# Performance work log

Measured on AMD Instinct MI355X. Metric: run time of the kernel, lower is better.

Reference implementation:

```python
import jax, jax.numpy as jnp
import numpy as np

EMBED_DIM = 768
NUM_HEADS = 12
HEAD_DIM = EMBED_DIM // NUM_HEADS


def setup_inputs() -> dict:
    key = jax.random.key(0)
    k1, k2, k3 = jax.random.split(key, 3)
    B, T = 128, 128
    x = jax.random.normal(k1, (B, T, EMBED_DIM), dtype=jnp.float32)
    # weights stored as [in, out] so forward is x @ W (equivalent to torch Linear, bias=False)
    w_qkv = jax.random.normal(k2, (EMBED_DIM, 3 * EMBED_DIM), dtype=jnp.float32) * (EMBED_DIM ** -0.5)
    w_proj = jax.random.normal(k3, (EMBED_DIM, EMBED_DIM), dtype=jnp.float32) * (EMBED_DIM ** -0.5)
    return {"x": x, "w_qkv": w_qkv, "w_proj": w_proj}


def reference(x, w_qkv, w_proj):
    B, T, C = x.shape
    # fused QKV projection -> (3, B, H, T, D)
    qkv = (x @ w_qkv).reshape(B, T, 3, NUM_HEADS, HEAD_DIM)
    q, k, v = jnp.transpose(qkv, (2, 0, 3, 1, 4))
    # scaled dot-product scores (B, H, T, T)
    att = jnp.einsum('bhqd,bhkd->bhqk', q, k) * (HEAD_DIM ** -0.5)
    causal = jnp.tril(jnp.ones((T, T), dtype=bool))
    att = jnp.where(causal, att, -jnp.inf)
    # float32 softmax then cast back (matches att.float().softmax().to(x.dtype))
    att = jax.nn.softmax(att.astype(jnp.float32), axis=-1).astype(x.dtype)
    # dropout is identity in eval/reference mode
    out = jnp.einsum('bhqk,bhkd->bhqd', att, v)          # (B, H, T, D)
    out = jnp.transpose(out, (0, 2, 1, 3)).reshape(B, T, C)
    return out @ w_proj
```

## Files before the change

kernel.cpp:

```cpp
#include <hip/hip_runtime.h>

typedef __bf16 bf16_t;
typedef bf16_t bf16x8 __attribute__((ext_vector_type(8)));
typedef bf16_t bf16x4 __attribute__((ext_vector_type(4)));
typedef float f32x4 __attribute__((ext_vector_type(4)));

__device__ __forceinline__ f32x4 mfma16(bf16x8 a, bf16x8 b, f32x4 c) {
  return __builtin_amdgcn_mfma_f32_16x16x32_bf16(a, b, c, 0, 0, 0);
}

__device__ __forceinline__ void gload16(const bf16_t* g, bf16_t* l) {
  __builtin_amdgcn_global_load_lds(
      (const __attribute__((address_space(1))) void*)g,
      (__attribute__((address_space(3))) void*)l, 16, 0, 0);
}

__global__ void prep_kernel(const float* __restrict__ x, const float* __restrict__ wq,
                            const float* __restrict__ wp, bf16_t* __restrict__ xb,
                            bf16_t* __restrict__ wqt, bf16_t* __restrict__ wpt) {
  __shared__ bf16_t tile[32][33];
  const int bid = blockIdx.x;
  if (bid < 12288) {
    int i = bid * 256 + threadIdx.x;
    float4 v = ((const float4*)x)[i];
    bf16x4 o;
    o[0] = (bf16_t)v.x; o[1] = (bf16_t)v.y; o[2] = (bf16_t)v.z; o[3] = (bf16_t)v.w;
    *(bf16x4*)&xb[(size_t)i * 4] = o;
    return;
  }
  const int t = bid - 12288;
  const int ty = t / 96, txb = t % 96;
  const float* in;
  bf16_t* out;
  int N, n0;
  if (txb < 72) { in = wq; out = wqt; N = 2304; n0 = txb * 32; }
  else          { in = wp; out = wpt; N = 768;  n0 = (txb - 72) * 32; }
  const int k0 = ty * 32;
  const int tx = threadIdx.x & 31, tyy = threadIdx.x >> 5;
#pragma unroll
  for (int ph = 0; ph < 4; ++ph) {
    int k = tyy + ph * 8;
    tile[k][tx] = (bf16_t)in[(size_t)(k0 + k) * N + n0 + tx];
  }
  __syncthreads();
#pragma unroll
  for (int ph = 0; ph < 4; ++ph) {
    int n = tyy + ph * 8;
    out[(size_t)(n0 + n) * 768 + k0 + tx] = tile[tx][n];
  }
}

template <int BN, bool F32OUT>
__global__ __launch_bounds__(256, 3) void gemm_persist(
    const bf16_t* __restrict__ A, const bf16_t* __restrict__ Bt,
    void* __restrict__ Cout, int N, int K, int nbn, int q, int r) {
  constexpr int NQ = BN / 32;
  __shared__ bf16_t As[2][128 * 64];
  __shared__ bf16_t Bs[2][BN * 64];
  const int tid = threadIdx.x;
  const int lane = tid & 63;
  const int w = tid >> 6;
  const int wm = w >> 1, wn = w & 1;
  const int lr = lane & 15, kg = lane >> 4;

  const int G = gridDim.x;
  const int bid = blockIdx.x;
  const int lb = (bid & 7) * (G >> 3) + (bid >> 3);
  int nj, start;
  if (lb < r) { nj = q + 1; start = lb * (q + 1); }
  else        { nj = q;     start = r * (q + 1) + (lb - r) * q; }

  const int NKT = K >> 6;
  const int sr = tid >> 3, sslot = tid & 7;

  auto stage = [&](int buf, const bf16_t* Aj, const bf16_t* Bj, int k0) {
#pragma unroll
    for (int it = 0; it < 4; ++it) {
      int rr = it * 32 + sr;
      gload16(Aj + (size_t)rr * K + (k0 + ((sslot ^ (rr & 7)) << 3)),
              &As[buf][(it * 256 + tid) * 8]);
    }
#pragma unroll
    for (int it = 0; it < NQ; ++it) {
      int rr = it * 32 + sr;
      gload16(Bj + (size_t)rr * K + (k0 + ((sslot ^ (rr & 7)) << 3)),
              &Bs[buf][(it * 256 + tid) * 8]);
    }
  };

  int job = start;
  int bm = job / nbn, bn = job % nbn;
  const bf16_t* Aj = A + (size_t)bm * 128 * K;
  const bf16_t* Bj = Bt + (size_t)bn * BN * K;
  stage(0, Aj, Bj, 0);
  __syncthreads();
  int buf = 0;

  for (int j = 0; j < nj; ++j) {
    f32x4 acc[4][NQ];
#pragma unroll
    for (int i = 0; i < 4; ++i)
#pragma unroll
      for (int n = 0; n < NQ; ++n) acc[i][n] = (f32x4){0.f, 0.f, 0.f, 0.f};

    int nbm = 0, nbnx = 0;
    const bf16_t *nAj = nullptr, *nBj = nullptr;
    if (j + 1 < nj) {
      int njob = job + 1;
      nbm = njob / nbn; nbnx = njob % nbn;
      nAj = A + (size_t)nbm * 128 * K;
      nBj = Bt + (size_t)nbnx * BN * K;
    }

    for (int kt = 0; kt < NKT; ++kt) {
      if (kt + 1 < NKT)      stage(buf ^ 1, Aj, Bj, (kt + 1) << 6);
      else if (j + 1 < nj)   stage(buf ^ 1, nAj, nBj, 0);
#pragma unroll
      for (int kk = 0; kk < 2; ++kk) {
        const int slot = ((kk << 2) + kg) ^ (lr & 7);
        bf16x8 af[4], bfv[NQ];
#pragma unroll
        for (int mq = 0; mq < 4; ++mq) {
          int rr = wm * 64 + mq * 16 + lr;
          af[mq] = *(const bf16x8*)&As[buf][(rr << 6) + (slot << 3)];
        }
#pragma unroll
        for (int nq = 0; nq < NQ; ++nq) {
          int rr = wn * (BN / 2) + nq * 16 + lr;
          bfv[nq] = *(const bf16x8*)&Bs[buf][(rr << 6) + (slot << 3)];
        }
#pragma unroll
        for (int mq = 0; mq < 4; ++mq)
#pragma unroll
          for (int nq = 0; nq < NQ; ++nq)
            acc[mq][nq] = mfma16(af[mq], bfv[nq], acc[mq][nq]);
      }
      __syncthreads();
      buf ^= 1;
    }

    const int row0 = bm * 128 + wm * 64 + kg * 4;
    const int col0 = bn * BN + wn * (BN / 2) + lr;
#pragma unroll
    for (int mq = 0; mq < 4; ++mq)
#pragma unroll
      for (int nq = 0; nq < NQ; ++nq)
#pragma unroll
        for (int rr = 0; rr < 4; ++rr) {
          size_t idx = (size_t)(row0 + mq * 16 + rr) * N + (col0 + nq * 16);
          if constexpr (F32OUT)
            ((float*)Cout)[idx] = acc[mq][nq][rr];
          else
            ((bf16_t*)Cout)[idx] = (bf16_t)acc[mq][nq][rr];
        }

    job++; bm = nbm; bn = nbnx; Aj = nAj; Bj = nBj;
  }
}

#define ATT_H 12
__global__ __launch_bounds__(256, 2) void attn_kernel(const bf16_t* __restrict__ qkv,
                                                      bf16_t* __restrict__ obuf) {
  __shared__ bf16_t Ks[128 * 72];
  __shared__ bf16_t Vt[64 * 136];
  __shared__ bf16_t Ps[128 * 136];
  const int tid = threadIdx.x, lane = tid & 63, w = tid >> 6;
  const int lr = lane & 15, kg = lane >> 4;
  const int bh = blockIdx.x;
  const int b = bh / ATT_H, h = bh % ATT_H;
  const size_t base = (size_t)b * 128 * 2304;
  const int hoff = h * 64;

#pragma unroll
  for (int it = 0; it < 4; ++it) {
    int idx = it * 256 + tid;
    int r = idx >> 3, slot = idx & 7;
    bf16x8 v = *(const bf16x8*)&qkv[base + (size_t)r * 2304 + 768 + hoff + slot * 8];
    *(bf16x8*)&Ks[r * 72 + slot * 8] = v;
  }
#pragma unroll 4
  for (int it = 0; it < 32; ++it) {
    int idx = it * 256 + tid;
    int t = idx >> 6, d = idx & 63;
    Vt[d * 136 + t] = qkv[base + (size_t)t * 2304 + 1536 + hoff + d];
  }
  const int qrow0 = w * 32;
  bf16x8 qf[2][2];
#pragma unroll
  for (int mt = 0; mt < 2; ++mt)
#pragma unroll
    for (int kk = 0; kk < 2; ++kk)
      qf[mt][kk] = *(const bf16x8*)&qkv[base + (size_t)(qrow0 + mt * 16 + lr) * 2304 + hoff +
                                        kk * 32 + kg * 8];
  __syncthreads();

  const int NT = 2 * w + 2;
  f32x4 acc[2][8];
#pragma unroll
  for (int mt = 0; mt < 2; ++mt)
#pragma unroll
    for (int nt = 0; nt < 8; ++nt) acc[mt][nt] = (f32x4){0.f, 0.f, 0.f, 0.f};

#pragma unroll
  for (int nt = 0; nt < 8; ++nt) {
    if (nt < NT) {
#pragma unroll
      for (int kk = 0; kk < 2; ++kk) {
        bf16x8 kf = *(const bf16x8*)&Ks[(nt * 16 + lr) * 72 + kk * 32 + kg * 8];
        acc[0][nt] = mfma16(qf[0][kk], kf, acc[0][nt]);
        acc[1][nt] = mfma16(qf[1][kk], kf, acc[1][nt]);
      }
    }
  }

#pragma unroll
  for (int mt = 0; mt < 2; ++mt) {
#pragma unroll
    for (int rr = 0; rr < 4; ++rr) {
      const int row = qrow0 + mt * 16 + kg * 4 + rr;
      float m = -1e30f;
#pragma unroll
      for (int nt = 0; nt < 8; ++nt) {
        if (nt < NT) {
          int col = nt * 16 + lr;
          float s = acc[mt][nt][rr] * 0.125f;
          s = (col <= row) ? s : -1e30f;
          acc[mt][nt][rr] = s;
          m = fmaxf(m, s);
        }
      }
      m = fmaxf(m, __shfl_xor(m, 1));
      m = fmaxf(m, __shfl_xor(m, 2));
      m = fmaxf(m, __shfl_xor(m, 4));
      m = fmaxf(m, __shfl_xor(m, 8));
      float ssum = 0.f;
#pragma unroll
      for (int nt = 0; nt < 8; ++nt) {
        if (nt < NT) {
          float p = __builtin_amdgcn_exp2f((acc[mt][nt][rr] - m) * 1.44269504f);
          acc[mt][nt][rr] = p;
          ssum += p;
        }
      }
      ssum += __shfl_xor(ssum, 1);
      ssum += __shfl_xor(ssum, 2);
      ssum += __shfl_xor(ssum, 4);
      ssum += __shfl_xor(ssum, 8);
      float inv = 1.0f / ssum;
#pragma unroll
      for (int nt = 0; nt < 8; ++nt) {
        if (nt < NT) Ps[row * 136 + nt * 16 + lr] = (bf16_t)(acc[mt][nt][rr] * inv);
      }
    }
  }

  f32x4 oacc[2][4];
#pragma unroll
  for (int mt = 0; mt < 2; ++mt)
#pragma unroll
    for (int dt = 0; dt < 4; ++dt) oacc[mt][dt] = (f32x4){0.f, 0.f, 0.f, 0.f};

  const int KS = w + 1;
#pragma unroll
  for (int ks = 0; ks < 4; ++ks) {
    if (ks < KS) {
      bf16x8 pa0 = *(const bf16x8*)&Ps[(qrow0 + lr) * 136 + ks * 32 + kg * 8];
      bf16x8 pa1 = *(const bf16x8*)&Ps[(qrow0 + 16 + lr) * 136 + ks * 32 + kg * 8];
#pragma unroll
      for (int dt = 0; dt < 4; ++dt) {
        bf16x8 vb = *(const bf16x8*)&Vt[(dt * 16 + lr) * 136 + ks * 32 + kg * 8];
        oacc[0][dt] = mfma16(pa0, vb, oacc[0][dt]);
        oacc[1][dt] = mfma16(pa1, vb, oacc[1][dt]);
      }
    }
  }

#pragma unroll
  for (int mt = 0; mt < 2; ++mt)
#pragma unroll
    for (int dt = 0; dt < 4; ++dt)
#pragma unroll
      for (int rr = 0; rr < 4; ++rr) {
        int t = qrow0 + mt * 16 + kg * 4 + rr;
        obuf[((size_t)b * 128 + t) * 768 + hoff + dt * 16 + lr] = (bf16_t)oacc[mt][dt][rr];
      }
}

extern "C" void kernel_launch(void* const* d_in, const int* in_sizes, int n_in,
                              void* d_out, int out_size, void* d_ws, size_t ws_size,
                              hipStream_t stream) {
  const float* x = (const float*)d_in[0];
  const float* w_qkv = (const float*)d_in[1];
  const float* w_proj = (const float*)d_in[2];
  float* out = (float*)d_out;
  char* ws = (char*)d_ws;

  bf16_t* xb     = (bf16_t*)(ws);
  bf16_t* wqkvt  = (bf16_t*)(ws + 25165824);
  bf16_t* wprojt = (bf16_t*)(ws + 28704768);
  bf16_t* qkv    = (bf16_t*)(ws + 29884416);
  bf16_t* obuf   = (bf16_t*)(ws + 105381888);

  prep_kernel<<<dim3(12288 + 2304), dim3(256), 0, stream>>>(x, w_qkv, w_proj, xb, wqkvt, wprojt);
  gemm_persist<128, false><<<dim3(512), dim3(256), 0, stream>>>(
      xb, wqkvt, (void*)qkv, 2304, 768, 18, 4, 256);
  attn_kernel<<<dim3(1536), dim3(256), 0, stream>>>(qkv, obuf);
  gemm_persist<64, true><<<dim3(768), dim3(256), 0, stream>>>(
      obuf, wprojt, (void*)out, 768, 768, 12, 2, 0);
}
```

Before: 157.9 us.

## Replace double-buffered GEMMs with 3-stage LDS ring and per-block A-row reuse

Both GEMMs now use a single kernel with a three-slot LDS ring buffer and a prefetch distance of two stages. The loads are tracked with explicit vmcnt waits and a single barrier per k-step, replacing the two syncthreads of the previous double buffer. Each block keeps one 128-row A panel and walks several consecutive 64-wide N tiles, so A stays cache-resident and the job schedule is simpler. The QKV GEMM changes from 128-wide to 64-wide N tiles, and occupancy drops to 2 blocks per CU. This trades fewer barriers and deeper prefetch for lower per-tile B reuse.

```diff
diff --git a/kernel.cpp b/kernel.cpp
--- a/kernel.cpp
+++ b/kernel.cpp
@@ -14,6 +14,14 @@
       (const __attribute__((address_space(1))) void*)g,
       (__attribute__((address_space(3))) void*)l, 16, 0, 0);
 }
+
+#define BARRIER()                      \
+  do {                                 \
+    asm volatile("" ::: "memory");     \
+    __builtin_amdgcn_s_barrier();      \
+    asm volatile("" ::: "memory");     \
+  } while (0)
+#define VMCNT(n) asm volatile("s_waitcnt vmcnt(" #n ")" ::: "memory")
 
 __global__ void prep_kernel(const float* __restrict__ x, const float* __restrict__ wq,
                             const float* __restrict__ wp, bf16_t* __restrict__ xb,
@@ -50,13 +58,13 @@
   }
 }
 
-template <int BN, bool F32OUT>
-__global__ __launch_bounds__(256, 3) void gemm_persist(
+template <bool F32OUT>
+__global__ __launch_bounds__(256, 2) void gemm_ring(
     const bf16_t* __restrict__ A, const bf16_t* __restrict__ Bt,
-    void* __restrict__ Cout, int N, int K, int nbn, int q, int r) {
-  constexpr int NQ = BN / 32;
-  __shared__ bf16_t As[2][128 * 64];
-  __shared__ bf16_t Bs[2][BN * 64];
+    void* __restrict__ Cout, int N, int nbn, int jpb) {
+  constexpr int K = 768;
+  constexpr int NKT = 12;
+  __shared__ bf16_t ring[3][12288];
   const int tid = threadIdx.x;
   const int lane = tid & 63;
   const int w = tid >> 6;
@@ -66,85 +74,82 @@
   const int G = gridDim.x;
   const int bid = blockIdx.x;
   const int lb = (bid & 7) * (G >> 3) + (bid >> 3);
-  int nj, start;
-  if (lb < r) { nj = q + 1; start = lb * (q + 1); }
-  else        { nj = q;     start = r * (q + 1) + (lb - r) * q; }
-
-  const int NKT = K >> 6;
-  const int sr = tid >> 3, sslot = tid & 7;
-
-  auto stage = [&](int buf, const bf16_t* Aj, const bf16_t* Bj, int k0) {
+  const int start = lb * jpb;
+  const int bm = start / nbn;
+  const int bn0 = start % nbn;
+  const bf16_t* Ab = A + (size_t)bm * 128 * K;
+  const int S = jpb * NKT;
+
+  auto stageS = [&](int s) {
+    if (s >= S) return;
+    const int jb = s / NKT;
+    const int kt = s - jb * NKT;
+    const int k0 = kt << 6;
+    const bf16_t* Bj = Bt + (size_t)(bn0 + jb) * 64 * K;
+    bf16_t* L = &ring[kt % 3][0];
 #pragma unroll
     for (int it = 0; it < 4; ++it) {
-      int rr = it * 32 + sr;
-      gload16(Aj + (size_t)rr * K + (k0 + ((sslot ^ (rr & 7)) << 3)),
-              &As[buf][(it * 256 + tid) * 8]);
-    }
-#pragma unroll
-    for (int it = 0; it < NQ; ++it) {
-      int rr = it * 32 + sr;
-      gload16(Bj + (size_t)rr * K + (k0 + ((sslot ^ (rr & 7)) << 3)),
-              &Bs[buf][(it * 256 + tid) * 8]);
+      int c = it * 256 + tid;
+      int r = c >> 3, p = c & 7;
+      gload16(Ab + (size_t)r * K + (k0 + ((p ^ (r & 7)) << 3)), L + c * 8);
+    }
+#pragma unroll
+    for (int it = 0; it < 2; ++it) {
+      int c = it * 256 + tid;
+      int r = c >> 3, p = c & 7;
+      gload16(Bj + (size_t)r * K + (k0 + ((p ^ (r & 7)) << 3)), L + 8192 + c * 8);
     }
   };
 
-  int job = start;
-  int bm = job / nbn, bn = job % nbn;
-  const bf16_t* Aj = A + (size_t)bm * 128 * K;
-  const bf16_t* Bj = Bt + (size_t)bn * BN * K;
-  stage(0, Aj, Bj, 0);
-  __syncthreads();
-  int buf = 0;
-
-  for (int j = 0; j < nj; ++j) {
-    f32x4 acc[4][NQ];
+  stageS(0);
+  stageS(1);
+
+  for (int j = 0; j < jpb; ++j) {
+    f32x4 acc[4][2];
 #pragma unroll
     for (int i = 0; i < 4; ++i)
 #pragma unroll
-      for (int n = 0; n < NQ; ++n) acc[i][n] = (f32x4){0.f, 0.f, 0.f, 0.f};
-
-    int nbm = 0, nbnx = 0;
-    const bf16_t *nAj = nullptr, *nBj = nullptr;
-    if (j + 1 < nj) {
-      int njob = job + 1;
-      nbm = njob / nbn; nbnx = njob % nbn;
-      nAj = A + (size_t)nbm * 128 * K;
-      nBj = Bt + (size_t)nbnx * BN * K;
-    }
+      for (int n = 0; n < 2; ++n) acc[i][n] = (f32x4){0.f, 0.f, 0.f, 0.f};
+
+    const int sbase = j * NKT;
+    const bool lastj = (j == jpb - 1);
 
     for (int kt = 0; kt < NKT; ++kt) {
-      if (kt + 1 < NKT)      stage(buf ^ 1, Aj, Bj, (kt + 1) << 6);
-      else if (j + 1 < nj)   stage(buf ^ 1, nAj, nBj, 0);
+      if (lastj && kt == NKT - 1) { VMCNT(0); } else { VMCNT(6); }
+      BARRIER();
+      stageS(sbase + kt + 2);
+
+      const bf16_t* L = &ring[kt % 3][0];
 #pragma unroll
       for (int kk = 0; kk < 2; ++kk) {
-        const int slot = ((kk << 2) + kg) ^ (lr & 7);
-        bf16x8 af[4], bfv[NQ];
+        const int q = (kk << 2) + kg;
+        const int ph = q ^ (lr & 7);
+        bf16x8 af[4], bfv[2];
 #pragma unroll
         for (int mq = 0; mq < 4; ++mq) {
-          int rr = wm * 64 + mq * 16 + lr;
-          af[mq] = *(const bf16x8*)&As[buf][(rr << 6) + (slot << 3)];
-        }
-#pragma unroll
-        for (int nq = 0; nq < NQ; ++nq) {
-          int rr = wn * (BN / 2) + nq * 16 + lr;
-          bfv[nq] = *(const bf16x8*)&Bs[buf][(rr << 6) + (slot << 3)];
+          int r = wm * 64 + mq * 16 + lr;
+          af[mq] = *(const bf16x8*)&L[r * 64 + ph * 8];
+        }
+#pragma unroll
+        for (int nq = 0; nq < 2; ++nq) {
+          int r = wn * 32 + nq * 16 + lr;
+          bfv[nq] = *(const bf16x8*)&L[8192 + r * 64 + ph * 8];
         }
 #pragma unroll
         for (int mq = 0; mq < 4; ++mq)
 #pragma unroll
-          for (int nq = 0; nq < NQ; ++nq)
+          for (int nq = 0; nq < 2; ++nq)
             acc[mq][nq] = mfma16(af[mq], bfv[nq], acc[mq][nq]);
       }
-      __syncthreads();
-      buf ^= 1;
-    }
-
+    }
+
+    const int bn = bn0 + j;
     const int row0 = bm * 128 + wm * 64 + kg * 4;
-    const int col0 = bn * BN + wn * (BN / 2) + lr;
+    const int col0 = bn * 64 + wn * 32 + lr;
 #pragma unroll
     for (int mq = 0; mq < 4; ++mq)
 #pragma unroll
-      for (int nq = 0; nq < NQ; ++nq)
+      for (int nq = 0; nq < 2; ++nq)
 #pragma unroll
         for (int rr = 0; rr < 4; ++rr) {
           size_t idx = (size_t)(row0 + mq * 16 + rr) * N + (col0 + nq * 16);
@@ -153,8 +158,6 @@
           else
             ((bf16_t*)Cout)[idx] = (bf16_t)acc[mq][nq][rr];
         }
-
-    job++; bm = nbm; bn = nbnx; Aj = nAj; Bj = nBj;
   }
 }
 
@@ -302,9 +305,7 @@
   bf16_t* obuf   = (bf16_t*)(ws + 105381888);
 
   prep_kernel<<<dim3(12288 + 2304), dim3(256), 0, stream>>>(x, w_qkv, w_proj, xb, wqkvt, wprojt);
-  gemm_persist<128, false><<<dim3(512), dim3(256), 0, stream>>>(
-      xb, wqkvt, (void*)qkv, 2304, 768, 18, 4, 256);
+  gemm_ring<false><<<dim3(512), dim3(256), 0, stream>>>(xb, wqkvt, (void*)qkv, 2304, 36, 9);
   attn_kernel<<<dim3(1536), dim3(256), 0, stream>>>(qkv, obuf);
-  gemm_persist<64, true><<<dim3(768), dim3(256), 0, stream>>>(
-      obuf, wprojt, (void*)out, 768, 768, 12, 2, 0);
-}
+  gemm_ring<true><<<dim3(512), dim3(256), 0, stream>>>(obuf, wprojt, (void*)out, 768, 12, 3);
+}
```

Result: no change. 157.2 us (-0.4%).

## Replace syncthreads with raw barriers and vmcnt waits in persistent GEMMs

Applied to the files above, without the earlier changes.

Both persistent GEMMs now use a flat step counter over jobs and k-tiles. Each step issues the next stage's async global-to-LDS loads between raw s_barrier calls and waits only on the older batch through an explicit vmcnt count, instead of relying on __syncthreads to drain everything. The intent is to let the prefetch overlap the MFMA work and to cut the full memory drain at each k-step. K is also made a compile-time constant, and the QKV GEMM's occupancy hint drops from 3 to 2 blocks per CU. The hand-written vmcnt values assume exact load counts per stage, and two barriers per step add sync overhead.

```diff
diff --git a/kernel.cpp b/kernel.cpp
--- a/kernel.cpp
+++ b/kernel.cpp
@@ -14,6 +14,14 @@
       (const __attribute__((address_space(1))) void*)g,
       (__attribute__((address_space(3))) void*)l, 16, 0, 0);
 }
+
+#define BARRIER()                      \
+  do {                                 \
+    asm volatile("" ::: "memory");     \
+    __builtin_amdgcn_s_barrier();      \
+    asm volatile("" ::: "memory");     \
+  } while (0)
+#define VMCNT(n) asm volatile("s_waitcnt vmcnt(" #n ")" ::: "memory")
 
 __global__ void prep_kernel(const float* __restrict__ x, const float* __restrict__ wq,
                             const float* __restrict__ wp, bf16_t* __restrict__ xb,
@@ -50,10 +58,12 @@
   }
 }
 
-template <int BN, bool F32OUT>
-__global__ __launch_bounds__(256, 3) void gemm_persist(
+template <int BN, int MAXB, bool F32OUT>
+__global__ __launch_bounds__(256, MAXB) void gemm_cnt(
     const bf16_t* __restrict__ A, const bf16_t* __restrict__ Bt,
-    void* __restrict__ Cout, int N, int K, int nbn, int q, int r) {
+    void* __restrict__ Cout, int N, int nbn, int q, int r) {
+  constexpr int K = 768;
+  constexpr int NKT = 12;
   constexpr int NQ = BN / 32;
   __shared__ bf16_t As[2][128 * 64];
   __shared__ bf16_t Bs[2][BN * 64];
@@ -69,11 +79,20 @@
   int nj, start;
   if (lb < r) { nj = q + 1; start = lb * (q + 1); }
   else        { nj = q;     start = r * (q + 1) + (lb - r) * q; }
-
-  const int NKT = K >> 6;
+  const int S = nj * NKT;
+
   const int sr = tid >> 3, sslot = tid & 7;
 
-  auto stage = [&](int buf, const bf16_t* Aj, const bf16_t* Bj, int k0) {
+  auto stageS = [&](int s) {
+    if (s >= S) return;
+    const int jb = s / NKT;
+    const int kt = s - jb * NKT;
+    const int job = start + jb;
+    const int bm = job / nbn, bn = job - bm * nbn;
+    const bf16_t* Aj = A + (size_t)bm * (128 * K);
+    const bf16_t* Bj = Bt + (size_t)bn * (BN * K);
+    const int k0 = kt << 6;
+    const int buf = s & 1;
 #pragma unroll
     for (int it = 0; it < 4; ++it) {
       int rr = it * 32 + sr;
@@ -88,13 +107,8 @@
     }
   };
 
-  int job = start;
-  int bm = job / nbn, bn = job % nbn;
-  const bf16_t* Aj = A + (size_t)bm * 128 * K;
-  const bf16_t* Bj = Bt + (size_t)bn * BN * K;
-  stage(0, Aj, Bj, 0);
-  __syncthreads();
-  int buf = 0;
+  stageS(0);
+  int s = 0;
 
   for (int j = 0; j < nj; ++j) {
     f32x4 acc[4][NQ];
@@ -103,18 +117,19 @@
 #pragma unroll
       for (int n = 0; n < NQ; ++n) acc[i][n] = (f32x4){0.f, 0.f, 0.f, 0.f};
 
-    int nbm = 0, nbnx = 0;
-    const bf16_t *nAj = nullptr, *nBj = nullptr;
-    if (j + 1 < nj) {
-      int njob = job + 1;
-      nbm = njob / nbn; nbnx = njob % nbn;
-      nAj = A + (size_t)nbm * 128 * K;
-      nBj = Bt + (size_t)nbnx * BN * K;
-    }
-
-    for (int kt = 0; kt < NKT; ++kt) {
-      if (kt + 1 < NKT)      stage(buf ^ 1, Aj, Bj, (kt + 1) << 6);
-      else if (j + 1 < nj)   stage(buf ^ 1, nAj, nBj, 0);
+    const int job = start + j;
+    const int bm = job / nbn, bn = job - bm * nbn;
+
+    for (int kt = 0; kt < NKT; ++kt, ++s) {
+      BARRIER();
+      stageS(s + 1);
+      if (s + 1 < S) {
+        if constexpr (BN == 128) { VMCNT(8); } else { VMCNT(6); }
+      } else {
+        VMCNT(0);
+      }
+      BARRIER();
+      const int buf = s & 1;
 #pragma unroll
       for (int kk = 0; kk < 2; ++kk) {
         const int slot = ((kk << 2) + kg) ^ (lr & 7);
@@ -135,8 +150,6 @@
           for (int nq = 0; nq < NQ; ++nq)
             acc[mq][nq] = mfma16(af[mq], bfv[nq], acc[mq][nq]);
       }
-      __syncthreads();
-      buf ^= 1;
     }
 
     const int row0 = bm * 128 + wm * 64 + kg * 4;
@@ -153,8 +166,6 @@
           else
             ((bf16_t*)Cout)[idx] = (bf16_t)acc[mq][nq][rr];
         }
-
-    job++; bm = nbm; bn = nbnx; Aj = nAj; Bj = nBj;
   }
 }
 
@@ -223,10 +234,10 @@
       for (int nt = 0; nt < 8; ++nt) {
         if (nt < NT) {
           int col = nt * 16 + lr;
-          float s = acc[mt][nt][rr] * 0.125f;
-          s = (col <= row) ? s : -1e30f;
-          acc[mt][nt][rr] = s;
-          m = fmaxf(m, s);
+          float sv = acc[mt][nt][rr] * 0.125f;
+          sv = (col <= row) ? sv : -1e30f;
+          acc[mt][nt][rr] = sv;
+          m = fmaxf(m, sv);
         }
       }
       m = fmaxf(m, __shfl_xor(m, 1));
@@ -302,9 +313,9 @@
   bf16_t* obuf   = (bf16_t*)(ws + 105381888);
 
   prep_kernel<<<dim3(12288 + 2304), dim3(256), 0, stream>>>(x, w_qkv, w_proj, xb, wqkvt, wprojt);
-  gemm_persist<128, false><<<dim3(512), dim3(256), 0, stream>>>(
-      xb, wqkvt, (void*)qkv, 2304, 768, 18, 4, 256);
+  gemm_cnt<128, 2, false><<<dim3(512), dim3(256), 0, stream>>>(
+      xb, wqkvt, (void*)qkv, 2304, 18, 4, 256);
   attn_kernel<<<dim3(1536), dim3(256), 0, stream>>>(qkv, obuf);
-  gemm_persist<64, true><<<dim3(768), dim3(256), 0, stream>>>(
-      obuf, wprojt, (void*)out, 768, 768, 12, 2, 0);
-}
+  gemm_cnt<64, 3, true><<<dim3(768), dim3(256), 0, stream>>>(
+      obuf, wprojt, (void*)out, 768, 12, 2, 0);
+}
```

Result: slower. 163.1 us (+3.3%).

## Halve GEMM k-tile to 32 to shrink LDS and raise occupancy

Applied to the files above, without the earlier changes.

The persistent GEMM now stages 32-wide K tiles instead of 64, with a new 4-slot XOR swizzle for the LDS layout. K is made a compile-time constant and the minimum waves per EU becomes a template parameter (3 for QKV, 6 for the output projection). The grids are enlarged so the QKV GEMM runs exactly 3 jobs per block and the projection GEMM runs 1. The smaller LDS footprint should let more blocks share a CU and hide latency better, at the cost of twice as many barriers and stage iterations per tile.

```diff
diff --git a/kernel.cpp b/kernel.cpp
--- a/kernel.cpp
+++ b/kernel.cpp
@@ -50,13 +50,15 @@
   }
 }
 
-template <int BN, bool F32OUT>
-__global__ __launch_bounds__(256, 3) void gemm_persist(
+template <int BN, int MINW, bool F32OUT>
+__global__ __launch_bounds__(256, MINW) void gemm_p32(
     const bf16_t* __restrict__ A, const bf16_t* __restrict__ Bt,
-    void* __restrict__ Cout, int N, int K, int nbn, int q, int r) {
+    void* __restrict__ Cout, int N, int nbn, int q, int r) {
+  constexpr int K = 768;
+  constexpr int NKT = 24;
   constexpr int NQ = BN / 32;
-  __shared__ bf16_t As[2][128 * 64];
-  __shared__ bf16_t Bs[2][BN * 64];
+  __shared__ bf16_t As[2][128 * 32];
+  __shared__ bf16_t Bs[2][BN * 32];
   const int tid = threadIdx.x;
   const int lane = tid & 63;
   const int w = tid >> 6;
@@ -70,31 +72,32 @@
   if (lb < r) { nj = q + 1; start = lb * (q + 1); }
   else        { nj = q;     start = r * (q + 1) + (lb - r) * q; }
 
-  const int NKT = K >> 6;
-  const int sr = tid >> 3, sslot = tid & 7;
-
   auto stage = [&](int buf, const bf16_t* Aj, const bf16_t* Bj, int k0) {
 #pragma unroll
-    for (int it = 0; it < 4; ++it) {
-      int rr = it * 32 + sr;
-      gload16(Aj + (size_t)rr * K + (k0 + ((sslot ^ (rr & 7)) << 3)),
-              &As[buf][(it * 256 + tid) * 8]);
-    }
-#pragma unroll
-    for (int it = 0; it < NQ; ++it) {
-      int rr = it * 32 + sr;
-      gload16(Bj + (size_t)rr * K + (k0 + ((sslot ^ (rr & 7)) << 3)),
-              &Bs[buf][(it * 256 + tid) * 8]);
+    for (int it = 0; it < 2; ++it) {
+      int c = it * 256 + tid;
+      int rr = c >> 2, p = c & 3;
+      gload16(Aj + (size_t)rr * K + (k0 + ((p ^ ((rr >> 1) & 3)) << 3)),
+              &As[buf][c * 8]);
+    }
+#pragma unroll
+    for (int it = 0; it < BN / 64; ++it) {
+      int c = it * 256 + tid;
+      int rr = c >> 2, p = c & 3;
+      gload16(Bj + (size_t)rr * K + (k0 + ((p ^ ((rr >> 1) & 3)) << 3)),
+              &Bs[buf][c * 8]);
     }
   };
 
   int job = start;
-  int bm = job / nbn, bn = job % nbn;
-  const bf16_t* Aj = A + (size_t)bm * 128 * K;
-  const bf16_t* Bj = Bt + (size_t)bn * BN * K;
+  int bm = job / nbn, bn = job - bm * nbn;
+  const bf16_t* Aj = A + (size_t)bm * (128 * K);
+  const bf16_t* Bj = Bt + (size_t)bn * (BN * K);
   stage(0, Aj, Bj, 0);
   __syncthreads();
   int buf = 0;
+
+  const int ph = kg ^ ((lr >> 1) & 3);
 
   for (int j = 0; j < nj; ++j) {
     f32x4 acc[4][NQ];
@@ -107,34 +110,32 @@
     const bf16_t *nAj = nullptr, *nBj = nullptr;
     if (j + 1 < nj) {
       int njob = job + 1;
-      nbm = njob / nbn; nbnx = njob % nbn;
-      nAj = A + (size_t)nbm * 128 * K;
-      nBj = Bt + (size_t)nbnx * BN * K;
+      nbm = njob / nbn; nbnx = njob - nbm * nbn;
+      nAj = A + (size_t)nbm * (128 * K);
+      nBj = Bt + (size_t)nbnx * (BN * K);
     }
 
     for (int kt = 0; kt < NKT; ++kt) {
-      if (kt + 1 < NKT)      stage(buf ^ 1, Aj, Bj, (kt + 1) << 6);
-      else if (j + 1 < nj)   stage(buf ^ 1, nAj, nBj, 0);
-#pragma unroll
-      for (int kk = 0; kk < 2; ++kk) {
-        const int slot = ((kk << 2) + kg) ^ (lr & 7);
-        bf16x8 af[4], bfv[NQ];
-#pragma unroll
-        for (int mq = 0; mq < 4; ++mq) {
-          int rr = wm * 64 + mq * 16 + lr;
-          af[mq] = *(const bf16x8*)&As[buf][(rr << 6) + (slot << 3)];
-        }
-#pragma unroll
-        for (int nq = 0; nq < NQ; ++nq) {
-          int rr = wn * (BN / 2) + nq * 16 + lr;
-          bfv[nq] = *(const bf16x8*)&Bs[buf][(rr << 6) + (slot << 3)];
-        }
-#pragma unroll
-        for (int mq = 0; mq < 4; ++mq)
-#pragma unroll
-          for (int nq = 0; nq < NQ; ++nq)
-            acc[mq][nq] = mfma16(af[mq], bfv[nq], acc[mq][nq]);
-      }
+      if (kt + 1 < NKT)     stage(buf ^ 1, Aj, Bj, (kt + 1) << 5);
+      else if (j + 1 < nj)  stage(buf ^ 1, nAj, nBj, 0);
+
+      bf16x8 af[4], bfv[NQ];
+#pragma unroll
+      for (int mq = 0; mq < 4; ++mq) {
+        int rr = wm * 64 + mq * 16 + lr;
+        af[mq] = *(const bf16x8*)&As[buf][(rr << 5) + (ph << 3)];
+      }
+#pragma unroll
+      for (int nq = 0; nq < NQ; ++nq) {
+        int rr = wn * (BN / 2) + nq * 16 + lr;
+        bfv[nq] = *(const bf16x8*)&Bs[buf][(rr << 5) + (ph << 3)];
+      }
+#pragma unroll
+      for (int mq = 0; mq < 4; ++mq)
+#pragma unroll
+        for (int nq = 0; nq < NQ; ++nq)
+          acc[mq][nq] = mfma16(af[mq], bfv[nq], acc[mq][nq]);
+
       __syncthreads();
       buf ^= 1;
     }
@@ -223,10 +224,10 @@
       for (int nt = 0; nt < 8; ++nt) {
         if (nt < NT) {
           int col = nt * 16 + lr;
-          float s = acc[mt][nt][rr] * 0.125f;
-          s = (col <= row) ? s : -1e30f;
-          acc[mt][nt][rr] = s;
-          m = fmaxf(m, s);
+          float sv = acc[mt][nt][rr] * 0.125f;
+          sv = (col <= row) ? sv : -1e30f;
+          acc[mt][nt][rr] = sv;
+          m = fmaxf(m, sv);
         }
       }
       m = fmaxf(m, __shfl_xor(m, 1));
@@ -302,9 +303,9 @@
   bf16_t* obuf   = (bf16_t*)(ws + 105381888);
 
   prep_kernel<<<dim3(12288 + 2304), dim3(256), 0, stream>>>(x, w_qkv, w_proj, xb, wqkvt, wprojt);
-  gemm_persist<128, false><<<dim3(512), dim3(256), 0, stream>>>(
-      xb, wqkvt, (void*)qkv, 2304, 768, 18, 4, 256);
+  gemm_p32<128, 3, false><<<dim3(768), dim3(256), 0, stream>>>(
+      xb, wqkvt, (void*)qkv, 2304, 18, 3, 0);
   attn_kernel<<<dim3(1536), dim3(256), 0, stream>>>(qkv, obuf);
-  gemm_persist<64, true><<<dim3(768), dim3(256), 0, stream>>>(
-      obuf, wprojt, (void*)out, 768, 768, 12, 2, 0);
-}
+  gemm_p32<64, 6, true><<<dim3(1536), dim3(256), 0, stream>>>(
+      obuf, wprojt, (void*)out, 768, 12, 1, 0);
+}
```

Result: slower. 162.9 us (+3.2%).
